# Kernel tuning notes

Hardware: AMD Instinct MI355X
Metric: run time of the kernel (lower is better)

Reference implementation:

```python
import jax, jax.numpy as jnp
import numpy as np

T, N, H, I = 128, 1024, 512, 64


def _orthogonal(key, shape, dtype=jnp.float32):
    # mimic torch nn.init.orthogonal_ on a [rows, cols] matrix
    rows, cols = shape
    a = jax.random.normal(key, (max(rows, cols), min(rows, cols)), dtype=jnp.float32)
    q, r = jnp.linalg.qr(a)
    q = q * jnp.sign(jnp.diag(r))
    if rows < cols:
        q = q.T
    return q[:rows, :cols].astype(dtype)


def setup_inputs() -> dict:
    key = jax.random.key(0)
    k1, k2, k3, k4, k5, k6 = jax.random.split(key, 6)
    hxs = jax.random.normal(k1, (N, H), dtype=jnp.float32)
    gru_init = jax.random.normal(k2, (T * N, H), dtype=jnp.float32)
    masks = jax.random.uniform(k3, (T * N, 1), dtype=jnp.float32)
    prev_action_one_hot = jax.random.normal(k4, (T, N, I), dtype=jnp.float32)
    # GRUCell params: weight_ih [3H, I], weight_hh [3H, H] (orthogonal init), zero biases
    W_ih = _orthogonal(k5, (3 * H, I))
    W_hh = _orthogonal(k6, (3 * H, H))
    b_ih = jnp.zeros((3 * H,), dtype=jnp.float32)
    b_hh = jnp.zeros((3 * H,), dtype=jnp.float32)
    return {"hxs": hxs, "gru_init": gru_init, "masks": masks,
            "prev_action_one_hot": prev_action_one_hot,
            "W_ih": W_ih, "W_hh": W_hh, "b_ih": b_ih, "b_hh": b_hh}


def _gru_cell(x, h, W_ih, W_hh, b_ih, b_hh):
    # PyTorch GRUCell math; gate order in weights is r, z, n
    gi = x @ W_ih.T + b_ih          # [N, 3H]
    gh = h @ W_hh.T + b_hh          # [N, 3H]
    i_r, i_z, i_n = jnp.split(gi, 3, axis=-1)
    h_r, h_z, h_n = jnp.split(gh, 3, axis=-1)
    r = jax.nn.sigmoid(i_r + h_r)
    z = jax.nn.sigmoid(i_z + h_z)
    n = jnp.tanh(i_n + r * h_n)
    return (1.0 - z) * n + z * h


def reference(hxs, gru_init, masks, prev_action_one_hot, W_ih, W_hh, b_ih, b_hh):
    n = hxs.shape[0]
    t = gru_init.shape[0] // n
    m = masks.reshape(t, n, 1)
    # NOTE: the original computes hxs*m + gru_init*(1-m) per step but never uses it
    # (dead code), so gru_init does not enter the output.

    def step(h, inp):
        mi, xi = inp
        h_new = _gru_cell(xi * mi, h * mi, W_ih, W_hh, b_ih, b_hh)
        return h_new, h_new

    h_final, outs = jax.lax.scan(step, hxs, (m, prev_action_one_hot))
    x = outs.reshape(t * n, -1)
    return x, h_final
```

## Files before the change

kernel.cpp:

```cpp
#include <hip/hip_runtime.h>


#define T_STEPS 128
#define NBATCH  1024
#define HDIM    512
#define IDIM    64
#define KTOT    576

typedef _Float16 half8  __attribute__((ext_vector_type(8)));
typedef _Float16 half4  __attribute__((ext_vector_type(4)));
typedef float    floatx4 __attribute__((ext_vector_type(4)));

__global__ void prep_w_kernel(const float* __restrict__ Whh,
                              const float* __restrict__ Wih,
                              _Float16* __restrict__ W16) {
    int idx = blockIdx.x * 256 + threadIdx.x;
    if (idx >= 1536 * KTOT) return;
    int c = idx / KTOT;
    int k = idx - c * KTOT;
    float v = (k < HDIM) ? Whh[c * HDIM + k] : Wih[c * IDIM + (k - HDIM)];
    W16[idx] = (_Float16)v;
}

__global__ void prep_x_kernel(const float* __restrict__ pact,
                              const float* __restrict__ masks,
                              _Float16* __restrict__ x16) {
    int idx = blockIdx.x * 256 + threadIdx.x;
    if (idx >= T_STEPS * NBATCH * IDIM / 4) return;
    int e = idx * 4;
    float mk = masks[e >> 6];
    floatx4 v = *(const floatx4*)(pact + e);
    half4 h;
    h[0] = (_Float16)(v.x * mk);
    h[1] = (_Float16)(v.y * mk);
    h[2] = (_Float16)(v.z * mk);
    h[3] = (_Float16)(v.w * mk);
    *(half4*)(x16 + e) = h;
}

__global__ void prep_h_kernel(const float* __restrict__ hxs,
                              const float* __restrict__ masks,
                              _Float16* __restrict__ h16) {
    int idx = blockIdx.x * 256 + threadIdx.x;
    if (idx >= NBATCH * HDIM / 4) return;
    int e = idx * 4;
    float mk = masks[e >> 9];
    floatx4 v = *(const floatx4*)(hxs + e);
    half4 h;
    h[0] = (_Float16)(v.x * mk);
    h[1] = (_Float16)(v.y * mk);
    h[2] = (_Float16)(v.z * mk);
    h[3] = (_Float16)(v.w * mk);
    *(half4*)(h16 + e) = h;
}

__device__ __forceinline__ float sigmoidf_(float x) {
    return 1.0f / (1.0f + __expf(-x));
}

#define MFMA16(a, b, c) __builtin_amdgcn_mfma_f32_16x16x32_f16((a), (b), (c), 0, 0, 0)

__global__ __launch_bounds__(128, 1)
void gru_step_kernel(const float* __restrict__ h_prev,
                     const _Float16* __restrict__ h16,
                     const _Float16* __restrict__ x16,
                     const float* __restrict__ m_t,
                     const float* __restrict__ m_next,
                     const _Float16* __restrict__ W16,
                     const float* __restrict__ b_ih,
                     const float* __restrict__ b_hh,
                     float* __restrict__ out_x,
                     float* __restrict__ out_h,
                     _Float16* __restrict__ h16_next) {
    const int tid  = threadIdx.x;
    const int wave = tid >> 6;
    const int lane = tid & 63;
    const int n16  = lane & 15;
    const int q    = lane >> 4;
    const int rowbase = (blockIdx.x >> 4) * 64 + wave * 32;
    const int colbase = (blockIdx.x & 15) * 32;

    floatx4 acc_r[2][2], acc_z[2][2], acc_hn[2][2], acc_in[2][2];
#pragma unroll
    for (int rs = 0; rs < 2; ++rs)
#pragma unroll
        for (int cs = 0; cs < 2; ++cs) {
            acc_r[rs][cs]  = (floatx4){0.f, 0.f, 0.f, 0.f};
            acc_z[rs][cs]  = (floatx4){0.f, 0.f, 0.f, 0.f};
            acc_hn[rs][cs] = (floatx4){0.f, 0.f, 0.f, 0.f};
            acc_in[rs][cs] = (floatx4){0.f, 0.f, 0.f, 0.f};
        }

    const _Float16* hptr = h16 + (rowbase + n16) * HDIM + q * 8;
    const _Float16* wptr = W16 + (colbase + n16) * KTOT + q * 8;

#pragma unroll 4
    for (int kt = 0; kt < 16; ++kt) {
        half8 hf0 = *(const half8*)(hptr);
        half8 hf1 = *(const half8*)(hptr + 16 * HDIM);
        half8 wr0 = *(const half8*)(wptr);
        half8 wr1 = *(const half8*)(wptr + 16 * KTOT);
        half8 wz0 = *(const half8*)(wptr + HDIM * KTOT);
        half8 wz1 = *(const half8*)(wptr + (HDIM + 16) * KTOT);
        half8 wn0 = *(const half8*)(wptr + 2 * HDIM * KTOT);
        half8 wn1 = *(const half8*)(wptr + (2 * HDIM + 16) * KTOT);
        acc_r[0][0]  = MFMA16(wr0, hf0, acc_r[0][0]);
        acc_r[0][1]  = MFMA16(wr1, hf0, acc_r[0][1]);
        acc_r[1][0]  = MFMA16(wr0, hf1, acc_r[1][0]);
        acc_r[1][1]  = MFMA16(wr1, hf1, acc_r[1][1]);
        acc_z[0][0]  = MFMA16(wz0, hf0, acc_z[0][0]);
        acc_z[0][1]  = MFMA16(wz1, hf0, acc_z[0][1]);
        acc_z[1][0]  = MFMA16(wz0, hf1, acc_z[1][0]);
        acc_z[1][1]  = MFMA16(wz1, hf1, acc_z[1][1]);
        acc_hn[0][0] = MFMA16(wn0, hf0, acc_hn[0][0]);
        acc_hn[0][1] = MFMA16(wn1, hf0, acc_hn[0][1]);
        acc_hn[1][0] = MFMA16(wn0, hf1, acc_hn[1][0]);
        acc_hn[1][1] = MFMA16(wn1, hf1, acc_hn[1][1]);
        hptr += 32;
        wptr += 32;
    }

    const _Float16* xptr = x16 + (rowbase + n16) * IDIM + q * 8;
#pragma unroll
    for (int kt = 0; kt < 2; ++kt) {
        half8 hf0 = *(const half8*)(xptr);
        half8 hf1 = *(const half8*)(xptr + 16 * IDIM);
        half8 wr0 = *(const half8*)(wptr);
        half8 wr1 = *(const half8*)(wptr + 16 * KTOT);
        half8 wz0 = *(const half8*)(wptr + HDIM * KTOT);
        half8 wz1 = *(const half8*)(wptr + (HDIM + 16) * KTOT);
        half8 wn0 = *(const half8*)(wptr + 2 * HDIM * KTOT);
        half8 wn1 = *(const half8*)(wptr + (2 * HDIM + 16) * KTOT);
        acc_r[0][0]  = MFMA16(wr0, hf0, acc_r[0][0]);
        acc_r[0][1]  = MFMA16(wr1, hf0, acc_r[0][1]);
        acc_r[1][0]  = MFMA16(wr0, hf1, acc_r[1][0]);
        acc_r[1][1]  = MFMA16(wr1, hf1, acc_r[1][1]);
        acc_z[0][0]  = MFMA16(wz0, hf0, acc_z[0][0]);
        acc_z[0][1]  = MFMA16(wz1, hf0, acc_z[0][1]);
        acc_z[1][0]  = MFMA16(wz0, hf1, acc_z[1][0]);
        acc_z[1][1]  = MFMA16(wz1, hf1, acc_z[1][1]);
        acc_in[0][0] = MFMA16(wn0, hf0, acc_in[0][0]);
        acc_in[0][1] = MFMA16(wn1, hf0, acc_in[0][1]);
        acc_in[1][0] = MFMA16(wn0, hf1, acc_in[1][0]);
        acc_in[1][1] = MFMA16(wn1, hf1, acc_in[1][1]);
        xptr += 32;
        wptr += 32;
    }

#pragma unroll
    for (int rs = 0; rs < 2; ++rs) {
        const int i = rowbase + rs * 16 + n16;
        const float mtv = m_t[i];
        const float mnv = m_next ? m_next[i] : 0.0f;
#pragma unroll
        for (int cs = 0; cs < 2; ++cs) {
            const int c0 = colbase + cs * 16 + q * 4;
            floatx4 bir = *(const floatx4*)(b_ih + c0);
            floatx4 bhr = *(const floatx4*)(b_hh + c0);
            floatx4 biz = *(const floatx4*)(b_ih + HDIM + c0);
            floatx4 bhz = *(const floatx4*)(b_hh + HDIM + c0);
            floatx4 bin = *(const floatx4*)(b_ih + 2 * HDIM + c0);
            floatx4 bhn = *(const floatx4*)(b_hh + 2 * HDIM + c0);
            floatx4 hp4 = *(const floatx4*)(h_prev + (size_t)i * HDIM + c0);
            floatx4 hv;
#pragma unroll
            for (int r = 0; r < 4; ++r) {
                const float rg = sigmoidf_(acc_r[rs][cs][r] + bir[r] + bhr[r]);
                const float zg = sigmoidf_(acc_z[rs][cs][r] + biz[r] + bhz[r]);
                const float ng = tanhf(acc_in[rs][cs][r] + bin[r] +
                                       rg * (acc_hn[rs][cs][r] + bhn[r]));
                hv[r] = (1.0f - zg) * ng + zg * (hp4[r] * mtv);
            }
            *(floatx4*)(out_x + (size_t)i * HDIM + c0) = hv;
            if (out_h) *(floatx4*)(out_h + (size_t)i * HDIM + c0) = hv;
            if (m_next) {
                half4 hh;
                hh[0] = (_Float16)(hv[0] * mnv);
                hh[1] = (_Float16)(hv[1] * mnv);
                hh[2] = (_Float16)(hv[2] * mnv);
                hh[3] = (_Float16)(hv[3] * mnv);
                *(half4*)(h16_next + (size_t)i * HDIM + c0) = hh;
            }
        }
    }
}

extern "C" void kernel_launch(void* const* d_in, const int* in_sizes, int n_in,
                              void* d_out, int out_size, void* d_ws, size_t ws_size,
                              hipStream_t stream) {
    const float* hxs   = (const float*)d_in[0];
    const float* masks = (const float*)d_in[2];
    const float* pact  = (const float*)d_in[3];
    const float* W_ih  = (const float*)d_in[4];
    const float* W_hh  = (const float*)d_in[5];
    const float* b_ih  = (const float*)d_in[6];
    const float* b_hh  = (const float*)d_in[7];
    float* out = (float*)d_out;

    _Float16* W16  = (_Float16*)d_ws;
    _Float16* x16  = W16 + 1536 * KTOT;
    _Float16* h16a = x16 + (size_t)T_STEPS * NBATCH * IDIM;
    _Float16* h16b = h16a + (size_t)NBATCH * HDIM;

    const int wtot = 1536 * KTOT;
    prep_w_kernel<<<(wtot + 255) / 256, 256, 0, stream>>>(W_hh, W_ih, W16);
    const int xtot = T_STEPS * NBATCH * IDIM / 4;
    prep_x_kernel<<<(xtot + 255) / 256, 256, 0, stream>>>(pact, masks, x16);
    const int htot = NBATCH * HDIM / 4;
    prep_h_kernel<<<(htot + 255) / 256, 256, 0, stream>>>(hxs, masks, h16a);

    for (int t = 0; t < T_STEPS; ++t) {
        const float* h_prev =
            (t == 0) ? hxs : out + (size_t)(t - 1) * NBATCH * HDIM;
        const _Float16* hcur = (t & 1) ? h16b : h16a;
        _Float16* hnext      = (t & 1) ? h16a : h16b;
        const float* mnext =
            (t < T_STEPS - 1) ? masks + (size_t)(t + 1) * NBATCH : nullptr;
        float* out_x = out + (size_t)t * NBATCH * HDIM;
        float* out_h =
            (t == T_STEPS - 1) ? out + (size_t)T_STEPS * NBATCH * HDIM : nullptr;
        gru_step_kernel<<<256, 128, 0, stream>>>(
            h_prev, hcur, x16 + (size_t)t * NBATCH * IDIM,
            masks + (size_t)t * NBATCH, mnext, W16, b_ih, b_hh,
            out_x, out_h, hnext);
    }
}
```

Before: 2.368 ms.

## Fuse all GRU timesteps into one persistent kernel with per-row-group barriers

Result: slower. 2.614 ms (+10.4%).

```diff
diff --git a/kernel.cpp b/kernel.cpp
--- a/kernel.cpp
+++ b/kernel.cpp
@@ -6,6 +6,8 @@
 #define HDIM    512
 #define IDIM    64
 #define KTOT    576
+#define NGROUPS 32
+#define CTR_STRIDE 64
 
 typedef _Float16 half8  __attribute__((ext_vector_type(8)));
 typedef _Float16 half4  __attribute__((ext_vector_type(4)));
@@ -13,7 +15,11 @@
 
 __global__ void prep_w_kernel(const float* __restrict__ Whh,
                               const float* __restrict__ Wih,
-                              _Float16* __restrict__ W16) {
+                              _Float16* __restrict__ W16,
+                              int* __restrict__ cnt) {
+    if (blockIdx.x == 0) {
+        for (int i = threadIdx.x; i < NGROUPS * CTR_STRIDE; i += 256) cnt[i] = 0;
+    }
     int idx = blockIdx.x * 256 + threadIdx.x;
     if (idx >= 1536 * KTOT) return;
     int c = idx / KTOT;
@@ -60,127 +66,166 @@
 
 #define MFMA16(a, b, c) __builtin_amdgcn_mfma_f32_16x16x32_f16((a), (b), (c), 0, 0, 0)
 
-__global__ __launch_bounds__(128, 1)
-void gru_step_kernel(const float* __restrict__ h_prev,
-                     const _Float16* __restrict__ h16,
-                     const _Float16* __restrict__ x16,
-                     const float* __restrict__ m_t,
-                     const float* __restrict__ m_next,
+__global__ __launch_bounds__(256, 1)
+void gru_scan_kernel(const float* __restrict__ hxs,
+                     const _Float16* __restrict__ x16all,
+                     const float* __restrict__ masks,
                      const _Float16* __restrict__ W16,
                      const float* __restrict__ b_ih,
                      const float* __restrict__ b_hh,
-                     float* __restrict__ out_x,
-                     float* __restrict__ out_h,
-                     _Float16* __restrict__ h16_next) {
+                     float* __restrict__ out,
+                     _Float16* h16a,
+                     _Float16* h16b,
+                     int* cnt) {
     const int tid  = threadIdx.x;
     const int wave = tid >> 6;
     const int lane = tid & 63;
     const int n16  = lane & 15;
     const int q    = lane >> 4;
-    const int rowbase = (blockIdx.x >> 4) * 64 + wave * 32;
-    const int colbase = (blockIdx.x & 15) * 32;
-
-    floatx4 acc_r[2][2], acc_z[2][2], acc_hn[2][2], acc_in[2][2];
-#pragma unroll
-    for (int rs = 0; rs < 2; ++rs)
-#pragma unroll
-        for (int cs = 0; cs < 2; ++cs) {
-            acc_r[rs][cs]  = (floatx4){0.f, 0.f, 0.f, 0.f};
-            acc_z[rs][cs]  = (floatx4){0.f, 0.f, 0.f, 0.f};
-            acc_hn[rs][cs] = (floatx4){0.f, 0.f, 0.f, 0.f};
-            acc_in[rs][cs] = (floatx4){0.f, 0.f, 0.f, 0.f};
-        }
-
-    const _Float16* hptr = h16 + (rowbase + n16) * HDIM + q * 8;
-    const _Float16* wptr = W16 + (colbase + n16) * KTOT + q * 8;
-
-#pragma unroll 4
-    for (int kt = 0; kt < 16; ++kt) {
-        half8 hf0 = *(const half8*)(hptr);
-        half8 hf1 = *(const half8*)(hptr + 16 * HDIM);
-        half8 wr0 = *(const half8*)(wptr);
-        half8 wr1 = *(const half8*)(wptr + 16 * KTOT);
-        half8 wz0 = *(const half8*)(wptr + HDIM * KTOT);
-        half8 wz1 = *(const half8*)(wptr + (HDIM + 16) * KTOT);
-        half8 wn0 = *(const half8*)(wptr + 2 * HDIM * KTOT);
-        half8 wn1 = *(const half8*)(wptr + (2 * HDIM + 16) * KTOT);
-        acc_r[0][0]  = MFMA16(wr0, hf0, acc_r[0][0]);
-        acc_r[0][1]  = MFMA16(wr1, hf0, acc_r[0][1]);
-        acc_r[1][0]  = MFMA16(wr0, hf1, acc_r[1][0]);
-        acc_r[1][1]  = MFMA16(wr1, hf1, acc_r[1][1]);
-        acc_z[0][0]  = MFMA16(wz0, hf0, acc_z[0][0]);
-        acc_z[0][1]  = MFMA16(wz1, hf0, acc_z[0][1]);
-        acc_z[1][0]  = MFMA16(wz0, hf1, acc_z[1][0]);
-        acc_z[1][1]  = MFMA16(wz1, hf1, acc_z[1][1]);
-        acc_hn[0][0] = MFMA16(wn0, hf0, acc_hn[0][0]);
-        acc_hn[0][1] = MFMA16(wn1, hf0, acc_hn[0][1]);
-        acc_hn[1][0] = MFMA16(wn0, hf1, acc_hn[1][0]);
-        acc_hn[1][1] = MFMA16(wn1, hf1, acc_hn[1][1]);
-        hptr += 32;
-        wptr += 32;
+    const int rg   = (int)blockIdx.x >> 3;
+    const int rowbase = rg * 32;
+    const int colw    = ((int)blockIdx.x & 7) * 64 + wave * 16;
+    const int c0      = colw + q * 4;
+    int* const ctr = cnt + rg * CTR_STRIDE;
+
+    half8 wreg[18][3];
+#pragma unroll
+    for (int kt = 0; kt < 18; ++kt)
+#pragma unroll
+        for (int g = 0; g < 3; ++g)
+            wreg[kt][g] = *(const half8*)(W16 +
+                (size_t)(g * HDIM + colw + n16) * KTOT + kt * 32 + q * 8);
+
+    floatx4 br4, bz4, bin4, bhn4;
+    {
+        floatx4 a = *(const floatx4*)(b_ih + c0);
+        floatx4 b = *(const floatx4*)(b_hh + c0);
+        br4 = a + b;
+        a = *(const floatx4*)(b_ih + HDIM + c0);
+        b = *(const floatx4*)(b_hh + HDIM + c0);
+        bz4 = a + b;
+        bin4 = *(const floatx4*)(b_ih + 2 * HDIM + c0);
+        bhn4 = *(const floatx4*)(b_hh + 2 * HDIM + c0);
     }
 
-    const _Float16* xptr = x16 + (rowbase + n16) * IDIM + q * 8;
-#pragma unroll
-    for (int kt = 0; kt < 2; ++kt) {
-        half8 hf0 = *(const half8*)(xptr);
-        half8 hf1 = *(const half8*)(xptr + 16 * IDIM);
-        half8 wr0 = *(const half8*)(wptr);
-        half8 wr1 = *(const half8*)(wptr + 16 * KTOT);
-        half8 wz0 = *(const half8*)(wptr + HDIM * KTOT);
-        half8 wz1 = *(const half8*)(wptr + (HDIM + 16) * KTOT);
-        half8 wn0 = *(const half8*)(wptr + 2 * HDIM * KTOT);
-        half8 wn1 = *(const half8*)(wptr + (2 * HDIM + 16) * KTOT);
-        acc_r[0][0]  = MFMA16(wr0, hf0, acc_r[0][0]);
-        acc_r[0][1]  = MFMA16(wr1, hf0, acc_r[0][1]);
-        acc_r[1][0]  = MFMA16(wr0, hf1, acc_r[1][0]);
-        acc_r[1][1]  = MFMA16(wr1, hf1, acc_r[1][1]);
-        acc_z[0][0]  = MFMA16(wz0, hf0, acc_z[0][0]);
-        acc_z[0][1]  = MFMA16(wz1, hf0, acc_z[0][1]);
-        acc_z[1][0]  = MFMA16(wz0, hf1, acc_z[1][0]);
-        acc_z[1][1]  = MFMA16(wz1, hf1, acc_z[1][1]);
-        acc_in[0][0] = MFMA16(wn0, hf0, acc_in[0][0]);
-        acc_in[0][1] = MFMA16(wn1, hf0, acc_in[0][1]);
-        acc_in[1][0] = MFMA16(wn0, hf1, acc_in[1][0]);
-        acc_in[1][1] = MFMA16(wn1, hf1, acc_in[1][1]);
-        xptr += 32;
-        wptr += 32;
-    }
-
-#pragma unroll
-    for (int rs = 0; rs < 2; ++rs) {
-        const int i = rowbase + rs * 16 + n16;
-        const float mtv = m_t[i];
-        const float mnv = m_next ? m_next[i] : 0.0f;
-#pragma unroll
-        for (int cs = 0; cs < 2; ++cs) {
-            const int c0 = colbase + cs * 16 + q * 4;
-            floatx4 bir = *(const floatx4*)(b_ih + c0);
-            floatx4 bhr = *(const floatx4*)(b_hh + c0);
-            floatx4 biz = *(const floatx4*)(b_ih + HDIM + c0);
-            floatx4 bhz = *(const floatx4*)(b_hh + HDIM + c0);
-            floatx4 bin = *(const floatx4*)(b_ih + 2 * HDIM + c0);
-            floatx4 bhn = *(const floatx4*)(b_hh + 2 * HDIM + c0);
-            floatx4 hp4 = *(const floatx4*)(h_prev + (size_t)i * HDIM + c0);
+    const size_t hO0 = (size_t)(rowbase + n16) * HDIM + q * 8;
+    const size_t hO1 = hO0 + (size_t)16 * HDIM;
+    const size_t xO0 = (size_t)(rowbase + n16) * IDIM + q * 8;
+    const size_t xO1 = xO0 + (size_t)16 * IDIM;
+    const int i0 = rowbase + n16;
+    const int i1 = i0 + 16;
+    const size_t oO0 = (size_t)i0 * HDIM + c0;
+    const size_t oO1 = (size_t)i1 * HDIM + c0;
+
+    const _Float16* hcur = h16a;
+    _Float16* hnxt = h16b;
+    const float* hprev32 = hxs;
+
+#pragma unroll 1
+    for (int t = 0; t < T_STEPS; ++t) {
+        floatx4 accr0  = (floatx4){0.f, 0.f, 0.f, 0.f};
+        floatx4 accr1  = (floatx4){0.f, 0.f, 0.f, 0.f};
+        floatx4 accz0  = (floatx4){0.f, 0.f, 0.f, 0.f};
+        floatx4 accz1  = (floatx4){0.f, 0.f, 0.f, 0.f};
+        floatx4 acchn0 = (floatx4){0.f, 0.f, 0.f, 0.f};
+        floatx4 acchn1 = (floatx4){0.f, 0.f, 0.f, 0.f};
+        floatx4 accin0 = (floatx4){0.f, 0.f, 0.f, 0.f};
+        floatx4 accin1 = (floatx4){0.f, 0.f, 0.f, 0.f};
+
+#pragma unroll
+        for (int kt = 0; kt < 16; ++kt) {
+            half8 h0 = *(const half8*)(hcur + hO0 + kt * 32);
+            half8 h1 = *(const half8*)(hcur + hO1 + kt * 32);
+            accr0  = MFMA16(wreg[kt][0], h0, accr0);
+            accz0  = MFMA16(wreg[kt][1], h0, accz0);
+            acchn0 = MFMA16(wreg[kt][2], h0, acchn0);
+            accr1  = MFMA16(wreg[kt][0], h1, accr1);
+            accz1  = MFMA16(wreg[kt][1], h1, accz1);
+            acchn1 = MFMA16(wreg[kt][2], h1, acchn1);
+        }
+        const _Float16* xt = x16all + (size_t)t * NBATCH * IDIM;
+#pragma unroll
+        for (int kk = 0; kk < 2; ++kk) {
+            half8 x0 = *(const half8*)(xt + xO0 + kk * 32);
+            half8 x1 = *(const half8*)(xt + xO1 + kk * 32);
+            accr0  = MFMA16(wreg[16 + kk][0], x0, accr0);
+            accz0  = MFMA16(wreg[16 + kk][1], x0, accz0);
+            accin0 = MFMA16(wreg[16 + kk][2], x0, accin0);
+            accr1  = MFMA16(wreg[16 + kk][0], x1, accr1);
+            accz1  = MFMA16(wreg[16 + kk][1], x1, accz1);
+            accin1 = MFMA16(wreg[16 + kk][2], x1, accin1);
+        }
+
+        float* out_x = out + (size_t)t * NBATCH * HDIM;
+        {
+            const float mtv = masks[(size_t)t * NBATCH + i0];
+            floatx4 hp = *(const floatx4*)(hprev32 + oO0);
             floatx4 hv;
 #pragma unroll
             for (int r = 0; r < 4; ++r) {
-                const float rg = sigmoidf_(acc_r[rs][cs][r] + bir[r] + bhr[r]);
-                const float zg = sigmoidf_(acc_z[rs][cs][r] + biz[r] + bhz[r]);
-                const float ng = tanhf(acc_in[rs][cs][r] + bin[r] +
-                                       rg * (acc_hn[rs][cs][r] + bhn[r]));
-                hv[r] = (1.0f - zg) * ng + zg * (hp4[r] * mtv);
-            }
-            *(floatx4*)(out_x + (size_t)i * HDIM + c0) = hv;
-            if (out_h) *(floatx4*)(out_h + (size_t)i * HDIM + c0) = hv;
-            if (m_next) {
+                float rg_ = sigmoidf_(accr0[r] + br4[r]);
+                float zg = sigmoidf_(accz0[r] + bz4[r]);
+                float ng = tanhf(accin0[r] + bin4[r] + rg_ * (acchn0[r] + bhn4[r]));
+                hv[r] = (1.0f - zg) * ng + zg * (hp[r] * mtv);
+            }
+            *(floatx4*)(out_x + oO0) = hv;
+            if (t == T_STEPS - 1) {
+                *(floatx4*)(out + (size_t)T_STEPS * NBATCH * HDIM + oO0) = hv;
+            } else {
+                const float mnv = masks[(size_t)(t + 1) * NBATCH + i0];
                 half4 hh;
                 hh[0] = (_Float16)(hv[0] * mnv);
                 hh[1] = (_Float16)(hv[1] * mnv);
                 hh[2] = (_Float16)(hv[2] * mnv);
                 hh[3] = (_Float16)(hv[3] * mnv);
-                *(half4*)(h16_next + (size_t)i * HDIM + c0) = hh;
-            }
+                __hip_atomic_store((unsigned long long*)(hnxt + oO0),
+                                   __builtin_bit_cast(unsigned long long, hh),
+                                   __ATOMIC_RELAXED, __HIP_MEMORY_SCOPE_AGENT);
+            }
+        }
+        {
+            const float mtv = masks[(size_t)t * NBATCH + i1];
+            floatx4 hp = *(const floatx4*)(hprev32 + oO1);
+            floatx4 hv;
+#pragma unroll
+            for (int r = 0; r < 4; ++r) {
+                float rg_ = sigmoidf_(accr1[r] + br4[r]);
+                float zg = sigmoidf_(accz1[r] + bz4[r]);
+                float ng = tanhf(accin1[r] + bin4[r] + rg_ * (acchn1[r] + bhn4[r]));
+                hv[r] = (1.0f - zg) * ng + zg * (hp[r] * mtv);
+            }
+            *(floatx4*)(out_x + oO1) = hv;
+            if (t == T_STEPS - 1) {
+                *(floatx4*)(out + (size_t)T_STEPS * NBATCH * HDIM + oO1) = hv;
+            } else {
+                const float mnv = masks[(size_t)(t + 1) * NBATCH + i1];
+                half4 hh;
+                hh[0] = (_Float16)(hv[0] * mnv);
+                hh[1] = (_Float16)(hv[1] * mnv);
+                hh[2] = (_Float16)(hv[2] * mnv);
+                hh[3] = (_Float16)(hv[3] * mnv);
+                __hip_atomic_store((unsigned long long*)(hnxt + oO1),
+                                   __builtin_bit_cast(unsigned long long, hh),
+                                   __ATOMIC_RELAXED, __HIP_MEMORY_SCOPE_AGENT);
+            }
+        }
+
+        hprev32 = out_x;
+        { const _Float16* tmp = hcur; hcur = hnxt; hnxt = (_Float16*)tmp; }
+
+        if (t != T_STEPS - 1) {
+            __syncthreads();
+            if (tid == 0) {
+                __hip_atomic_fetch_add(ctr, 1, __ATOMIC_RELEASE,
+                                       __HIP_MEMORY_SCOPE_AGENT);
+                const int target = 8 * (t + 1);
+                while (__hip_atomic_load(ctr, __ATOMIC_RELAXED,
+                                         __HIP_MEMORY_SCOPE_AGENT) < target) {
+                    __builtin_amdgcn_s_sleep(1);
+                }
+            }
+            __syncthreads();
+            __builtin_amdgcn_fence(__ATOMIC_ACQUIRE, "agent");
         }
     }
 }
@@ -201,27 +246,15 @@
     _Float16* x16  = W16 + 1536 * KTOT;
     _Float16* h16a = x16 + (size_t)T_STEPS * NBATCH * IDIM;
     _Float16* h16b = h16a + (size_t)NBATCH * HDIM;
+    int* cnt       = (int*)(h16b + (size_t)NBATCH * HDIM);
 
     const int wtot = 1536 * KTOT;
-    prep_w_kernel<<<(wtot + 255) / 256, 256, 0, stream>>>(W_hh, W_ih, W16);
+    prep_w_kernel<<<(wtot + 255) / 256, 256, 0, stream>>>(W_hh, W_ih, W16, cnt);
     const int xtot = T_STEPS * NBATCH * IDIM / 4;
     prep_x_kernel<<<(xtot + 255) / 256, 256, 0, stream>>>(pact, masks, x16);
     const int htot = NBATCH * HDIM / 4;
     prep_h_kernel<<<(htot + 255) / 256, 256, 0, stream>>>(hxs, masks, h16a);
 
-    for (int t = 0; t < T_STEPS; ++t) {
-        const float* h_prev =
-            (t == 0) ? hxs : out + (size_t)(t - 1) * NBATCH * HDIM;
-        const _Float16* hcur = (t & 1) ? h16b : h16a;
-        _Float16* hnext      = (t & 1) ? h16a : h16b;
-        const float* mnext =
-            (t < T_STEPS - 1) ? masks + (size_t)(t + 1) * NBATCH : nullptr;
-        float* out_x = out + (size_t)t * NBATCH * HDIM;
-        float* out_h =
-            (t == T_STEPS - 1) ? out + (size_t)T_STEPS * NBATCH * HDIM : nullptr;
-        gru_step_kernel<<<256, 128, 0, stream>>>(
-            h_prev, hcur, x16 + (size_t)t * NBATCH * IDIM,
-            masks + (size_t)t * NBATCH, mnext, W16, b_ih, b_hh,
-            out_x, out_h, hnext);
-    }
-}
+    gru_scan_kernel<<<256, 256, 0, stream>>>(
+        hxs, x16, masks, W16, b_ih, b_hh, out, h16a, h16b, cnt);
+}
```
